# Performance work log

Hardware: AMD Instinct MI355X
Metric: run time of the kernel (lower is better)

## Reference

```python
import jax, jax.numpy as jnp
import numpy as np

LAYER_SIZES = [3, 3, 3]
CHANNELS = 192
BATCH = 65536
FULL_SIZES = [1] + LAYER_SIZES + [1]  # 1 -> 3 -> 3 -> 3 -> 1
NUM_LAYERS = len(LAYER_SIZES) + 1     # 4


def setup_inputs() -> dict:
    key = jax.random.key(0)
    ks = jax.random.split(key, 1 + len(LAYER_SIZES) + NUM_LAYERS + NUM_LAYERS)
    inp = {"x": jax.random.normal(ks[0], (BATCH, CHANNELS, 1), dtype=jnp.float32)}
    i = 1
    for k, sz in enumerate(LAYER_SIZES):
        inp[f"a{k}"] = jax.random.normal(ks[i], (CHANNELS, sz), dtype=jnp.float32); i += 1
    for k in range(NUM_LAYERS):  # b[k] has size full_sizes[k+1]
        inp[f"b{k}"] = jax.random.normal(ks[i], (CHANNELS, FULL_SIZES[k + 1]), dtype=jnp.float32); i += 1
    for k in range(NUM_LAYERS):
        inp[f"H{k}"] = jax.random.normal(ks[i], (CHANNELS, FULL_SIZES[k], FULL_SIZES[k + 1]), dtype=jnp.float32); i += 1
    return inp


def _cdf(x, a_list, b_list, H_list):
    # x: (B, C, 1)
    for k in range(NUM_LAYERS - 1):
        # per-channel matmul: (B,C,M) x (C,M,P) -> (B,C,P), with softplus-constrained H
        x = jnp.einsum('bni,nip->bnp', x, jax.nn.softplus(H_list[k])) + b_list[k]
        x = x + jnp.tanh(a_list[k]) * jnp.tanh(x)
    x = jnp.einsum('bni,nip->bnp', x, jax.nn.softplus(H_list[-1])) + b_list[-1]
    return jax.nn.sigmoid(x)


def reference(x, a0, a1, a2, b0, b1, b2, b3, H0, H1, H2, H3):
    a_list = [a0, a1, a2]
    b_list = [b0, b1, b2, b3]
    H_list = [H0, H1, H2, H3]
    # PDF of y_tilde: c(x + 1/2) - c(x - 1/2)
    half = jnp.asarray(0.5, dtype=x.dtype)
    p = _cdf(x + half, a_list, b_list, H_list) - _cdf(x - half, a_list, b_list, H_list)
    return p
```

## Files before the change

### kernel.cpp

```cpp
#include <hip/hip_runtime.h>
#include <hip/hip_bf16.h>
#include <math.h>

#define CHN 192
#define BATCHN 65536
#define NWS 61
#define CPB 64
#define NCG (CHN / CPB)
#define BLOCKT 256
#define RGROUPS 4
#define ROWS_PER_GROUP 16
#define ROWS_PER_BLOCK 64
#define RSLAB 4
#define NSLABS (ROWS_PER_GROUP / RSLAB)
#define NBLOCKS (NCG * (BATCHN / ROWS_PER_BLOCK))

#define KSCALE 2.885390081777926f
#define LOG2E  1.4426950408889634f

__device__ __forceinline__ float fast_rcp(float x)  { return __builtin_amdgcn_rcpf(x); }
__device__ __forceinline__ float fast_exp2(float x) { return __builtin_amdgcn_exp2f(x); }

__device__ __forceinline__ float softplus_acc(float h) {
    if (h > 20.0f) return h;
    return log1pf(expf(h));
}

__global__ __launch_bounds__(CHN) void weights_kernel(
    const float* __restrict__ a0, const float* __restrict__ a1, const float* __restrict__ a2,
    const float* __restrict__ b0, const float* __restrict__ b1, const float* __restrict__ b2,
    const float* __restrict__ b3,
    const float* __restrict__ H0, const float* __restrict__ H1, const float* __restrict__ H2,
    const float* __restrict__ H3,
    float* __restrict__ ws)
{
    const int c = threadIdx.x;
#pragma unroll
    for (int i = 0; i < 3; ++i) {
        float w0k = KSCALE * softplus_acc(H0[c * 3 + i]);
        float h   = 0.5f * w0k;
        float t1k0 = KSCALE * tanhf(a0[c * 3 + i]);
        ws[(0  + i) * CHN + c] = w0k;
        ws[(3  + i) * CHN + c] = KSCALE * b0[c * 3 + i];
        ws[(6  + i) * CHN + c] = exp2f(h);
        ws[(9  + i) * CHN + c] = exp2f(-h);
        ws[(12 + i) * CHN + c] = h + t1k0;
        ws[(15 + i) * CHN + c] = -h + t1k0;
        ws[(18 + i) * CHN + c] = -2.0f * t1k0;

        float t1k1 = KSCALE * tanhf(a1[c * 3 + i]);
        ws[(30 + i) * CHN + c] = KSCALE * b1[c * 3 + i];
        ws[(33 + i) * CHN + c] = t1k1;
        ws[(36 + i) * CHN + c] = -2.0f * t1k1;

        float t1k2 = KSCALE * tanhf(a2[c * 3 + i]);
        ws[(48 + i) * CHN + c] = KSCALE * b2[c * 3 + i];
        ws[(51 + i) * CHN + c] = t1k2;
        ws[(54 + i) * CHN + c] = -2.0f * t1k2;

        ws[(57 + i) * CHN + c] = -0.5f * softplus_acc(H3[c * 3 + i]);
    }
#pragma unroll
    for (int i = 0; i < 9; ++i) {
        ws[(21 + i) * CHN + c] = softplus_acc(H1[c * 9 + i]);
        ws[(39 + i) * CHN + c] = softplus_acc(H2[c * 9 + i]);
    }
    ws[60 * CHN + c] = -LOG2E * b3[c];
}

__global__ __launch_bounds__(BLOCKT, 4) void density_kernel(
    const float* __restrict__ x,
    const float* __restrict__ wt,
    float* __restrict__ out)
{
    __shared__ float sW[NWS * CPB];

    const int tid  = threadIdx.x;
    const int cb   = blockIdx.x % NCG;
    const int tile = blockIdx.x / NCG;

    {
        const float4* w4 = reinterpret_cast<const float4*>(wt);
        float4* s4 = reinterpret_cast<float4*>(sW);
        constexpr int NV = (NWS * CPB) / 4;
        for (int j = tid; j < NV; j += BLOCKT) {
            int s = j >> 4, v = j & 15;
            s4[j] = w4[(s * CHN + cb * CPB) / 4 + v];
        }
    }
    __syncthreads();

    const int cl = tid & (CPB - 1);
    const int g  = tid >> 6;
    const int cg = cb * CPB + cl;
    const int row0 = tile * ROWS_PER_BLOCK + g * ROWS_PER_GROUP;

    for (int sl = 0; sl < NSLABS; ++sl) {
        int off = 0;
        asm volatile("" : "+v"(off));
        const float* Wl = sW + cl + off;
#define WS(s) Wl[(s) * CPB]

        const int base = (row0 + sl * RSLAB) * CHN + cg;
        float xv[RSLAB];
#pragma unroll
        for (int r = 0; r < RSLAB; ++r) xv[r] = x[base + r * CHN];

        float vp[RSLAB][3], vm[RSLAB][3];
#pragma unroll
        for (int i = 0; i < 3; ++i) {
            float w0k = WS(0 + i),  b0k = WS(3 + i);
            float cp  = WS(6 + i),  cm  = WS(9 + i);
            float gp  = WS(12 + i), gm  = WS(15 + i), t2 = WS(18 + i);
#pragma unroll
            for (int r = 0; r < RSLAB; ++r) {
                float q  = fmaf(w0k, xv[r], b0k);
                float E  = fast_exp2(q);
                float rp = fast_rcp(fmaf(E, cp, 1.0f));
                float rm = fast_rcp(fmaf(E, cm, 1.0f));
                vp[r][i] = fmaf(t2, rp, q + gp);
                vm[r][i] = fmaf(t2, rm, q + gm);
            }
        }
        float zp[RSLAB][3], zm[RSLAB][3];
#pragma unroll
        for (int p = 0; p < 3; ++p) {
            float w0 = WS(21 + p), w1 = WS(24 + p), w2 = WS(27 + p);
            float bb = WS(30 + p), t1 = WS(33 + p), t2 = WS(36 + p);
#pragma unroll
            for (int r = 0; r < RSLAB; ++r) {
                float tp = fmaf(vp[r][2], w2, fmaf(vp[r][1], w1, fmaf(vp[r][0], w0, bb)));
                float tm = fmaf(vm[r][2], w2, fmaf(vm[r][1], w1, fmaf(vm[r][0], w0, bb)));
                float rp = fast_rcp(fast_exp2(tp) + 1.0f);
                float rm = fast_rcp(fast_exp2(tm) + 1.0f);
                zp[r][p] = fmaf(t2, rp, tp + t1);
                zm[r][p] = fmaf(t2, rm, tm + t1);
            }
        }
        float yp[RSLAB][3], ym[RSLAB][3];
#pragma unroll
        for (int p = 0; p < 3; ++p) {
            float w0 = WS(39 + p), w1 = WS(42 + p), w2 = WS(45 + p);
            float bb = WS(48 + p), t1 = WS(51 + p), t2 = WS(54 + p);
#pragma unroll
            for (int r = 0; r < RSLAB; ++r) {
                float tp = fmaf(zp[r][2], w2, fmaf(zp[r][1], w1, fmaf(zp[r][0], w0, bb)));
                float tm = fmaf(zm[r][2], w2, fmaf(zm[r][1], w1, fmaf(zm[r][0], w0, bb)));
                float rp = fast_rcp(fast_exp2(tp) + 1.0f);
                float rm = fast_rcp(fast_exp2(tm) + 1.0f);
                yp[r][p] = fmaf(t2, rp, tp + t1);
                ym[r][p] = fmaf(t2, rm, tm + t1);
            }
        }
        {
            float w30 = WS(57), w31 = WS(58), w32 = WS(59), b3n = WS(60);
#pragma unroll
            for (int r = 0; r < RSLAB; ++r) {
                float sp = fmaf(yp[r][2], w32, fmaf(yp[r][1], w31, fmaf(yp[r][0], w30, b3n)));
                float sm = fmaf(ym[r][2], w32, fmaf(ym[r][1], w31, fmaf(ym[r][0], w30, b3n)));
                float pp = fast_rcp(fast_exp2(sp) + 1.0f);
                float pm = fast_rcp(fast_exp2(sm) + 1.0f);
                out[base + r * CHN] = pp - pm;
            }
        }
#undef WS
    }
}

extern "C" void kernel_launch(void* const* d_in, const int* in_sizes, int n_in,
                              void* d_out, int out_size, void* d_ws, size_t ws_size,
                              hipStream_t stream) {
    const float* x  = (const float*)d_in[0];
    const float* a0 = (const float*)d_in[1];
    const float* a1 = (const float*)d_in[2];
    const float* a2 = (const float*)d_in[3];
    const float* b0 = (const float*)d_in[4];
    const float* b1 = (const float*)d_in[5];
    const float* b2 = (const float*)d_in[6];
    const float* b3 = (const float*)d_in[7];
    const float* H0 = (const float*)d_in[8];
    const float* H1 = (const float*)d_in[9];
    const float* H2 = (const float*)d_in[10];
    const float* H3 = (const float*)d_in[11];
    float* out = (float*)d_out;
    float* ws  = (float*)d_ws;

    weights_kernel<<<1, CHN, 0, stream>>>(a0, a1, a2, b0, b1, b2, b3,
                                          H0, H1, H2, H3, ws);
    density_kernel<<<NBLOCKS, BLOCKT, 0, stream>>>(x, ws, out);
}
```

Measured before the change: 77.73 us.

## Fold tanh offset into bias and prefetch next slab of inputs

Layers 1 and 2 now have the tanh shift t1 folded into the bias, with exp2(-t1) precomputed as a multiplier inside the sigmoid. This removes one add per element in each hidden layer. The kernel also issues the global loads for the next row slab before computing the current one, and loads the first slab before the shared-memory weight staging, so load latency overlaps with compute. The cost is extra live registers for the prefetched values, which could hurt occupancy.

```diff
diff --git a/kernel.cpp b/kernel.cpp
--- a/kernel.cpp
+++ b/kernel.cpp
@@ -8,7 +8,6 @@
 #define CPB 64
 #define NCG (CHN / CPB)
 #define BLOCKT 256
-#define RGROUPS 4
 #define ROWS_PER_GROUP 16
 #define ROWS_PER_BLOCK 64
 #define RSLAB 4
@@ -49,13 +48,13 @@
         ws[(18 + i) * CHN + c] = -2.0f * t1k0;
 
         float t1k1 = KSCALE * tanhf(a1[c * 3 + i]);
-        ws[(30 + i) * CHN + c] = KSCALE * b1[c * 3 + i];
-        ws[(33 + i) * CHN + c] = t1k1;
+        ws[(30 + i) * CHN + c] = KSCALE * b1[c * 3 + i] + t1k1;
+        ws[(33 + i) * CHN + c] = exp2f(-t1k1);
         ws[(36 + i) * CHN + c] = -2.0f * t1k1;
 
         float t1k2 = KSCALE * tanhf(a2[c * 3 + i]);
-        ws[(48 + i) * CHN + c] = KSCALE * b2[c * 3 + i];
-        ws[(51 + i) * CHN + c] = t1k2;
+        ws[(48 + i) * CHN + c] = KSCALE * b2[c * 3 + i] + t1k2;
+        ws[(51 + i) * CHN + c] = exp2f(-t1k2);
         ws[(54 + i) * CHN + c] = -2.0f * t1k2;
 
         ws[(57 + i) * CHN + c] = -0.5f * softplus_acc(H3[c * 3 + i]);
@@ -78,6 +77,18 @@
     const int tid  = threadIdx.x;
     const int cb   = blockIdx.x % NCG;
     const int tile = blockIdx.x / NCG;
+
+    const int cl = tid & (CPB - 1);
+    const int g  = tid >> 6;
+    const int cg = cb * CPB + cl;
+    const int row0 = tile * ROWS_PER_BLOCK + g * ROWS_PER_GROUP;
+
+    float xv[RSLAB];
+    {
+        const int base0 = row0 * CHN + cg;
+#pragma unroll
+        for (int r = 0; r < RSLAB; ++r) xv[r] = x[base0 + r * CHN];
+    }
 
     {
         const float4* w4 = reinterpret_cast<const float4*>(wt);
@@ -90,21 +101,20 @@
     }
     __syncthreads();
 
-    const int cl = tid & (CPB - 1);
-    const int g  = tid >> 6;
-    const int cg = cb * CPB + cl;
-    const int row0 = tile * ROWS_PER_BLOCK + g * ROWS_PER_GROUP;
-
     for (int sl = 0; sl < NSLABS; ++sl) {
+        float xnext[RSLAB];
+        if (sl + 1 < NSLABS) {
+            const int basen = (row0 + (sl + 1) * RSLAB) * CHN + cg;
+#pragma unroll
+            for (int r = 0; r < RSLAB; ++r) xnext[r] = x[basen + r * CHN];
+        }
+
         int off = 0;
         asm volatile("" : "+v"(off));
         const float* Wl = sW + cl + off;
 #define WS(s) Wl[(s) * CPB]
 
         const int base = (row0 + sl * RSLAB) * CHN + cg;
-        float xv[RSLAB];
-#pragma unroll
-        for (int r = 0; r < RSLAB; ++r) xv[r] = x[base + r * CHN];
 
         float vp[RSLAB][3], vm[RSLAB][3];
 #pragma unroll
@@ -126,30 +136,30 @@
 #pragma unroll
         for (int p = 0; p < 3; ++p) {
             float w0 = WS(21 + p), w1 = WS(24 + p), w2 = WS(27 + p);
-            float bb = WS(30 + p), t1 = WS(33 + p), t2 = WS(36 + p);
-#pragma unroll
-            for (int r = 0; r < RSLAB; ++r) {
-                float tp = fmaf(vp[r][2], w2, fmaf(vp[r][1], w1, fmaf(vp[r][0], w0, bb)));
-                float tm = fmaf(vm[r][2], w2, fmaf(vm[r][1], w1, fmaf(vm[r][0], w0, bb)));
-                float rp = fast_rcp(fast_exp2(tp) + 1.0f);
-                float rm = fast_rcp(fast_exp2(tm) + 1.0f);
-                zp[r][p] = fmaf(t2, rp, tp + t1);
-                zm[r][p] = fmaf(t2, rm, tm + t1);
+            float bb = WS(30 + p), c1 = WS(33 + p), t2 = WS(36 + p);
+#pragma unroll
+            for (int r = 0; r < RSLAB; ++r) {
+                float tq = fmaf(vp[r][2], w2, fmaf(vp[r][1], w1, fmaf(vp[r][0], w0, bb)));
+                float tn = fmaf(vm[r][2], w2, fmaf(vm[r][1], w1, fmaf(vm[r][0], w0, bb)));
+                float rp = fast_rcp(fmaf(fast_exp2(tq), c1, 1.0f));
+                float rm = fast_rcp(fmaf(fast_exp2(tn), c1, 1.0f));
+                zp[r][p] = fmaf(t2, rp, tq);
+                zm[r][p] = fmaf(t2, rm, tn);
             }
         }
         float yp[RSLAB][3], ym[RSLAB][3];
 #pragma unroll
         for (int p = 0; p < 3; ++p) {
             float w0 = WS(39 + p), w1 = WS(42 + p), w2 = WS(45 + p);
-            float bb = WS(48 + p), t1 = WS(51 + p), t2 = WS(54 + p);
-#pragma unroll
-            for (int r = 0; r < RSLAB; ++r) {
-                float tp = fmaf(zp[r][2], w2, fmaf(zp[r][1], w1, fmaf(zp[r][0], w0, bb)));
-                float tm = fmaf(zm[r][2], w2, fmaf(zm[r][1], w1, fmaf(zm[r][0], w0, bb)));
-                float rp = fast_rcp(fast_exp2(tp) + 1.0f);
-                float rm = fast_rcp(fast_exp2(tm) + 1.0f);
-                yp[r][p] = fmaf(t2, rp, tp + t1);
-                ym[r][p] = fmaf(t2, rm, tm + t1);
+            float bb = WS(48 + p), c1 = WS(51 + p), t2 = WS(54 + p);
+#pragma unroll
+            for (int r = 0; r < RSLAB; ++r) {
+                float tq = fmaf(zp[r][2], w2, fmaf(zp[r][1], w1, fmaf(zp[r][0], w0, bb)));
+                float tn = fmaf(zm[r][2], w2, fmaf(zm[r][1], w1, fmaf(zm[r][0], w0, bb)));
+                float rp = fast_rcp(fmaf(fast_exp2(tq), c1, 1.0f));
+                float rm = fast_rcp(fmaf(fast_exp2(tn), c1, 1.0f));
+                yp[r][p] = fmaf(t2, rp, tq);
+                ym[r][p] = fmaf(t2, rm, tn);
             }
         }
         {
@@ -164,6 +174,8 @@
             }
         }
 #undef WS
+#pragma unroll
+        for (int r = 0; r < RSLAB; ++r) xv[r] = xnext[r];
     }
 }
 
```

Measured after the change: 75.89 us. 2.4% less time.
